# Kernel optimization log

Hardware: AMD Instinct MI355X
Metric: run time of the kernel (lower is better)

## Reference

```python
import jax, jax.numpy as jnp
import numpy as np

K = 8  # search_range in sample_wise_recolor
BIG = 1e30


def setup_inputs() -> dict:
    key = jax.random.key(0)
    ks = jax.random.split(key, 6)
    L, N = 16384, 10000  # L: upsampled candidate voxels (multiple of 8), N: target points
    pred_F = jax.random.normal(ks[0], (L,), jnp.float32)
    cand_xyz = jax.random.normal(ks[1], (L, 3), jnp.float32) * 50.0
    cand_rgb = jax.random.uniform(ks[2], (L, 3), jnp.float32)
    tgt_xyz = jax.random.normal(ks[3], (N, 3), jnp.float32) * 50.0
    tgt_rgb = jax.random.uniform(ks[4], (N, 3), jnp.float32)
    keep_target = jax.random.randint(ks[5], (L,), 0, 2, jnp.int32)
    return {"pred_F": pred_F, "cand_xyz": cand_xyz, "cand_rgb": cand_rgb,
            "tgt_xyz": tgt_xyz, "tgt_rgb": tgt_rgb, "keep_target": keep_target,
            "points_num": 8192}


def _get_keep(pred, points_num):
    # local-max mask over groups of 8 children (scatter of per-row argmax)
    L = pred.shape[0]
    p8 = pred.reshape(-1, 8)
    rows = jnp.arange(p8.shape[0])
    is_local_max = jnp.zeros(p8.shape, dtype=bool).at[rows, jnp.argmax(p8, axis=1)].set(True).reshape(-1)
    # kthvalue over the non-local-max subset: local-max entries pushed to +inf so the
    # k-th smallest of the full sorted array equals the k-th smallest of the subset.
    k = L - points_num  # static python int
    vals = jnp.where(is_local_max, jnp.inf, pred)
    threshold = jnp.sort(vals)[k - 1]
    return (pred > threshold) | is_local_max


def _pairwise_sqdist(a, b):
    # a: [P,3], b: [Q,3] -> [P,Q] squared distances
    a2 = jnp.sum(a * a, axis=1)
    b2 = jnp.sum(b * b, axis=1)
    d2 = a2[:, None] + b2[None, :] - 2.0 * (a @ b.T)
    return jnp.maximum(d2, 0.0)


def _recolor_loss(cand_xyz, rgb, keep, tgt_xyz, tgt_rgb):
    L = cand_xyz.shape[0]
    N = tgt_xyz.shape[0]
    d2 = _pairwise_sqdist(tgt_xyz, cand_xyz)  # [N, L]

    # ---- recolor_backward: KNN from each target point into kept candidates ----
    d_masked = jnp.where(keep[None, :], d2, BIG)
    neg_d, idx = jax.lax.top_k(-d_masked, K)  # [N, K]
    d = -neg_d
    zero_mask = d == 0.0
    min_mask = (d == jnp.min(d, axis=1, keepdims=True)) & ~jnp.any(zero_mask, axis=1)[:, None]
    w = jnp.where(min_mask, 1.0 / jnp.sqrt(jnp.maximum(d, 1e-30)), 0.0)  # [N, K]

    flat_idx = idx.reshape(-1)
    num = jnp.zeros((L, 3), rgb.dtype).at[flat_idx].add((tgt_rgb[:, None, :] * w[:, :, None]).reshape(-1, 3))
    den = jnp.zeros((L,), rgb.dtype).at[flat_idx].add(w.reshape(-1))
    has_den = den != 0.0
    recolored = jnp.where(has_den[:, None], num / jnp.where(has_den, den, 1.0)[:, None], 0.0)

    # exact-match (zero-distance) targets overwrite; scatter with safe out-of-range dummy row
    safe_idx = jnp.where(zero_mask, idx, L).reshape(-1)
    tgt_exp = jnp.broadcast_to(tgt_rgb[:, None, :], (N, K, 3)).reshape(-1, 3)
    recolored = jnp.concatenate([recolored, jnp.zeros((1, 3), rgb.dtype)], 0).at[safe_idx].set(tgt_exp)[:L]
    empty = jnp.concatenate([~has_den, jnp.zeros((1,), bool)], 0).at[safe_idx].set(False)[:L]
    empty = empty & keep  # only kept candidates matter

    # ---- recolor_forward: kept candidates with no color yet pull from nearest targets ----
    neg_df, idxf = jax.lax.top_k(-d2.T, K)  # [L, K]
    df = -neg_df
    mf = df == jnp.min(df, axis=1, keepdims=True)
    rec_fwd = jnp.sum(tgt_rgb[idxf] * mf[:, :, None], axis=1) / jnp.sum(mf, axis=1, keepdims=True).astype(rgb.dtype)
    recolored = jnp.where(empty[:, None], rec_fwd, recolored)

    # L1 loss over kept candidates only; recolor target is no-grad in the original
    recolored = jax.lax.stop_gradient(recolored)
    return jnp.sum(jnp.where(keep[:, None], jnp.abs(rgb - recolored), 0.0))


def reference(pred_F, cand_xyz, cand_rgb, tgt_xyz, tgt_rgb, keep_target, points_num):
    keep = _get_keep(jax.lax.stop_gradient(pred_F), points_num)  # @torch.no_grad
    # coord recon loss: BCE-with-logits, reduction='sum'
    t = keep_target.astype(pred_F.dtype)
    coord_loss = jnp.sum(jnp.maximum(pred_F, 0.0) - pred_F * t + jnp.log1p(jnp.exp(-jnp.abs(pred_F))))
    # inverse_transform_for_color in training mode: x * 255
    rgb = cand_rgb * 255.0
    rgb_loss = _recolor_loss(cand_xyz, rgb, keep, tgt_xyz, tgt_rgb)
    return jnp.stack([coord_loss, rgb_loss])
```

## Files before the change

### kernel.cpp

```cpp
#include <hip/hip_runtime.h>
#include <hip/hip_bf16.h>


#define SCAN_T 256
typedef unsigned long long ull;

__global__ __launch_bounds__(256) void k_prep(
    const float* __restrict__ pred, const float* __restrict__ txyz,
    float4* __restrict__ ttile, float4* __restrict__ numden,
    int* __restrict__ zerohit, ull* __restrict__ tmin, ull* __restrict__ fmin,
    unsigned int* __restrict__ key, unsigned char* __restrict__ islm,
    int* __restrict__ counters, float* __restrict__ out, int L, int N) {
  int gidx = blockIdx.x * 256 + threadIdx.x;
  int gsz = (int)gridDim.x * 256;
  for (int i = gidx; i < N; i += gsz) {
    float x = txyz[3*i], y = txyz[3*i+1], z = txyz[3*i+2];
    ttile[i] = make_float4(x, y, z, fmaf(x, x, fmaf(y, y, z * z)));
    tmin[i] = ~0ull;
  }
  for (int i = gidx; i < L; i += gsz) {
    numden[i] = make_float4(0.f, 0.f, 0.f, 0.f);
    zerohit[i] = 0;
    fmin[i] = ~0ull;
  }
  if (gidx < 8) counters[gidx] = 0;
  if (gidx < 2) out[gidx] = 0.f;
  int ngroups = L >> 3;
  for (int g = gidx; g < ngroups; g += gsz) {
    const float4* pv = (const float4*)pred + (size_t)g * 2;
    float4 a = pv[0], b = pv[1];
    float v[8] = {a.x, a.y, a.z, a.w, b.x, b.y, b.z, b.w};
    int bi = 0; float bv = v[0];
    #pragma unroll
    for (int j = 1; j < 8; ++j) if (v[j] > bv) { bv = v[j]; bi = j; }
    unsigned int kk[8];
    ull lmpack = 0ull;
    #pragma unroll
    for (int j = 0; j < 8; ++j) {
      unsigned int fb = __float_as_uint(v[j]);
      unsigned int mk = (fb & 0x80000000u) ? ~fb : (fb | 0x80000000u);
      if (j == bi) { mk = 0xFF800000u; lmpack |= 1ull << (8 * j); }
      kk[j] = mk;
    }
    ((uint4*)key)[g*2]   = make_uint4(kk[0], kk[1], kk[2], kk[3]);
    ((uint4*)key)[g*2+1] = make_uint4(kk[4], kk[5], kk[6], kk[7]);
    *(ull*)(islm + (size_t)g * 8) = lmpack;
  }
}

__device__ __forceinline__ void select_bin(
    unsigned int* hist, int nb, unsigned int rank,
    unsigned int* sB, unsigned int* sR, int tid) {
  if (tid < 64) {
    int g = nb >> 6;
    unsigned int sum = 0;
    for (int j = 0; j < g; ++j) sum += hist[tid * g + j];
    unsigned int incl = sum;
    for (int o = 1; o < 64; o <<= 1) {
      unsigned int v = __shfl_up(incl, o);
      if (tid >= o) incl += v;
    }
    unsigned int excl = incl - sum;
    bool cond = (rank >= excl) && (rank < incl);
    unsigned long long bal = __ballot(cond);
    int first = __ffsll((long long)bal) - 1;
    if (tid == first) {
      unsigned int r = rank - excl, cum = 0;
      for (int j = 0; j < g; ++j) {
        unsigned int c = hist[tid * g + j];
        if (r < cum + c) { *sB = (unsigned int)(tid * g + j); *sR = r - cum; break; }
        cum += c;
      }
    }
  }
}

__global__ __launch_bounds__(256) void k_sel(
    const unsigned int* __restrict__ key, const int* __restrict__ pnum_p,
    float* __restrict__ thr_out, int L) {
  __shared__ unsigned int hist[2048];
  __shared__ unsigned int sB, sR;
  int tid = threadIdx.x;
  unsigned int rank = (unsigned int)(L - pnum_p[0] - 1);
  const uint4* k4 = (const uint4*)key;
  int n4 = L >> 2;
  for (int b = tid; b < 2048; b += 256) hist[b] = 0u;
  __syncthreads();
  for (int i = tid; i < n4; i += 256) {
    uint4 v = k4[i];
    atomicAdd(&hist[v.x >> 21], 1u); atomicAdd(&hist[v.y >> 21], 1u);
    atomicAdd(&hist[v.z >> 21], 1u); atomicAdd(&hist[v.w >> 21], 1u);
  }
  __syncthreads();
  select_bin(hist, 2048, rank, &sB, &sR, tid);
  __syncthreads();
  unsigned int B1 = sB, R1 = sR;
  for (int b = tid; b < 2048; b += 256) hist[b] = 0u;
  __syncthreads();
  for (int i = tid; i < n4; i += 256) {
    uint4 v = k4[i];
    if ((v.x >> 21) == B1) atomicAdd(&hist[(v.x >> 10) & 2047u], 1u);
    if ((v.y >> 21) == B1) atomicAdd(&hist[(v.y >> 10) & 2047u], 1u);
    if ((v.z >> 21) == B1) atomicAdd(&hist[(v.z >> 10) & 2047u], 1u);
    if ((v.w >> 21) == B1) atomicAdd(&hist[(v.w >> 10) & 2047u], 1u);
  }
  __syncthreads();
  select_bin(hist, 2048, R1, &sB, &sR, tid);
  __syncthreads();
  unsigned int B2 = sB, R2 = sR;
  for (int b = tid; b < 1024; b += 256) hist[b] = 0u;
  __syncthreads();
  unsigned int top22 = (B1 << 11) | B2;
  for (int i = tid; i < n4; i += 256) {
    uint4 v = k4[i];
    if ((v.x >> 10) == top22) atomicAdd(&hist[v.x & 1023u], 1u);
    if ((v.y >> 10) == top22) atomicAdd(&hist[v.y & 1023u], 1u);
    if ((v.z >> 10) == top22) atomicAdd(&hist[v.z & 1023u], 1u);
    if ((v.w >> 10) == top22) atomicAdd(&hist[v.w & 1023u], 1u);
  }
  __syncthreads();
  select_bin(hist, 1024, R2, &sB, &sR, tid);
  __syncthreads();
  if (tid == 0) {
    unsigned int fkey = (B1 << 21) | (B2 << 10) | sB;
    unsigned int fb = (fkey & 0x80000000u) ? (fkey & 0x7FFFFFFFu) : ~fkey;
    thr_out[0] = __uint_as_float(fb);
  }
}

__global__ __launch_bounds__(256) void k_keepc(
    const float* __restrict__ pred, const unsigned char* __restrict__ islm,
    const float* __restrict__ thr_p, const float* __restrict__ cxyz,
    const int* __restrict__ ktgt, int* __restrict__ keep,
    float4* __restrict__ klist, int* __restrict__ kidx,
    int* __restrict__ counters, float* __restrict__ out, int L) {
  int i = blockIdx.x * 256 + threadIdx.x;
  float thr = thr_p[0];
  float term = 0.f;
  if (i < L) {
    float p = pred[i];
    bool kp = (p > thr) || islm[i];
    keep[i] = kp ? 1 : 0;
    if (kp) {
      int pos = atomicAdd(&counters[0], 1);
      float x = cxyz[3*i], y = cxyz[3*i+1], z = cxyz[3*i+2];
      klist[pos] = make_float4(x, y, z, fmaf(x, x, fmaf(y, y, z * z)));
      kidx[pos] = i;
    }
    float t = (float)ktgt[i];
    term = fmaxf(p, 0.f) - p * t + log1pf(expf(-fabsf(p)));
  }
  for (int o = 32; o > 0; o >>= 1) term += __shfl_down(term, o);
  if ((threadIdx.x & 63) == 0) atomicAdd(&out[0], term);
}

__global__ __launch_bounds__(SCAN_T) void k_scan2(
    const float* __restrict__ txyz, const float4* __restrict__ klist,
    const int* __restrict__ kidx, const float4* __restrict__ ttile,
    const int* __restrict__ counters, ull* __restrict__ tmin,
    ull* __restrict__ fmin, int L, int N, int YB) {
  __shared__ float4 tile[SCAN_T];
  int tid = threadIdx.x, x = blockIdx.x, y = blockIdx.y;
  int kc = counters[0];

  if (y < YB) {
    int c0 = y * 512;
    if (x * 256 >= N || c0 >= kc) return;
    int c1 = min(c0 + 512, kc);
    int t = x * 256 + tid;
    bool act = t < N;
    float tx = 0.f, ty = 0.f, tz = 0.f;
    if (act) { tx = txyz[3*t]; ty = txyz[3*t+1]; tz = txyz[3*t+2]; }
    float ntx = -2.f * tx, nty = -2.f * ty, ntz = -2.f * tz;
    float best = 3e38f; int bpos = -1;
    for (int tb = c0; tb < c1; tb += SCAN_T) {
      int cnt = min(SCAN_T, c1 - tb);
      if (tid < cnt) tile[tid] = klist[tb + tid];
      __syncthreads();
      #pragma unroll 8
      for (int c = 0; c < cnt; ++c) {
        float4 cd = tile[c];
        float d = fmaf(ntx, cd.x, cd.w);
        d = fmaf(nty, cd.y, d);
        d = fmaf(ntz, cd.z, d);
        if (d < best) { best = d; bpos = tb + c; }
      }
      __syncthreads();
    }
    if (act && bpos >= 0) {
      float4 cd = klist[bpos];
      float dx = tx - cd.x, dy = ty - cd.y, dz = tz - cd.z;
      float dtrue = fmaf(dx, dx, fmaf(dy, dy, dz * dz));
      ull pack = ((ull)__float_as_uint(dtrue) << 32) | (unsigned int)kidx[bpos];
      atomicMin(&tmin[t], pack);
    }
  } else {
    int t0 = (y - YB) * 512;
    if (x * 256 >= kc) return;
    int t1 = min(t0 + 512, N);
    int e = x * 256 + tid;
    bool act = e < kc;
    float cx = 0.f, cy = 0.f, cz = 0.f, c2 = 0.f;
    int l = 0;
    if (act) {
      float4 cd = klist[e];
      cx = cd.x; cy = cd.y; cz = cd.z; c2 = cd.w;
      l = kidx[e];
    }
    float ncx = -2.f * cx, ncy = -2.f * cy, ncz = -2.f * cz;
    float best = 3e38f; int bidx = 0;
    for (int tb = t0; tb < t1; tb += SCAN_T) {
      int cnt = min(SCAN_T, t1 - tb);
      if (tid < cnt) tile[tid] = ttile[tb + tid];
      __syncthreads();
      #pragma unroll 8
      for (int c = 0; c < cnt; ++c) {
        float4 td = tile[c];
        float d = fmaf(ncx, td.x, td.w);
        d = fmaf(ncy, td.y, d);
        d = fmaf(ncz, td.z, d);
        if (d < best) { best = d; bidx = tb + c; }
      }
      __syncthreads();
    }
    if (act) {
      float dkey = fmaxf(best + c2, 0.f);
      ull pack = ((ull)__float_as_uint(dkey) << 32) | (unsigned int)bidx;
      atomicMin(&fmin[l], pack);
    }
  }
}

__global__ __launch_bounds__(256) void k_scatter(
    const float* __restrict__ trgb, const ull* __restrict__ tmin,
    float4* __restrict__ numden, int* __restrict__ zerohit,
    float4* __restrict__ zcolor, int N) {
  int t = blockIdx.x * 256 + threadIdx.x;
  if (t >= N) return;
  ull pack = tmin[t];
  float d = __uint_as_float((unsigned int)(pack >> 32));
  int idx = (int)(pack & 0xFFFFFFFFull);
  float r = trgb[3*t], g = trgb[3*t+1], b = trgb[3*t+2];
  if (d == 0.0f) {
    zerohit[idx] = 1;
    zcolor[idx] = make_float4(r, g, b, 0.f);
  } else {
    float w = 1.0f / sqrtf(fmaxf(d, 1e-30f));
    atomicAdd(&numden[idx].x, r * w);
    atomicAdd(&numden[idx].y, g * w);
    atomicAdd(&numden[idx].z, b * w);
    atomicAdd(&numden[idx].w, w);
  }
}

__global__ __launch_bounds__(256) void k_loss(
    const float* __restrict__ crgb, const float* __restrict__ trgb,
    const int* __restrict__ keep, const float4* __restrict__ numden,
    const int* __restrict__ zerohit, const float4* __restrict__ zcolor,
    const ull* __restrict__ fmin, float* __restrict__ out, int L) {
  int l = blockIdx.x * 256 + threadIdx.x;
  float loss = 0.f;
  if (l < L && keep[l]) {
    float rr, rg, rb;
    if (zerohit[l]) {
      float4 z = zcolor[l]; rr = z.x; rg = z.y; rb = z.z;
    } else {
      float4 nd = numden[l];
      if (nd.w != 0.f) { rr = nd.x / nd.w; rg = nd.y / nd.w; rb = nd.z / nd.w; }
      else {
        int ti = (int)(fmin[l] & 0xFFFFFFFFull);
        rr = trgb[3*ti]; rg = trgb[3*ti+1]; rb = trgb[3*ti+2];
      }
    }
    float sr = crgb[3*l]*255.f, sg = crgb[3*l+1]*255.f, sb = crgb[3*l+2]*255.f;
    loss = fabsf(sr - rr) + fabsf(sg - rg) + fabsf(sb - rb);
  }
  for (int o = 32; o > 0; o >>= 1) loss += __shfl_down(loss, o);
  if ((threadIdx.x & 63) == 0) atomicAdd(&out[1], loss);
}

extern "C" void kernel_launch(void* const* d_in, const int* in_sizes, int n_in,
                              void* d_out, int out_size, void* d_ws, size_t ws_size,
                              hipStream_t stream) {
  const float* pred = (const float*)d_in[0];
  const float* cxyz = (const float*)d_in[1];
  const float* crgb = (const float*)d_in[2];
  const float* txyz = (const float*)d_in[3];
  const float* trgb = (const float*)d_in[4];
  const int*   ktgt = (const int*)d_in[5];
  const int*   pnum = (const int*)d_in[6];
  int L = in_sizes[0];
  int N = in_sizes[3] / 3;

  char* ws = (char*)d_ws;
  size_t off = 0;
  float4* klist  = (float4*)(ws + off);   off += (size_t)L * 16;
  float4* ttile  = (float4*)(ws + off);   off += (size_t)((N + 3) & ~3) * 16;
  float4* numden = (float4*)(ws + off);   off += (size_t)L * 16;
  float4* zcolor = (float4*)(ws + off);   off += (size_t)L * 16;
  unsigned int* key = (unsigned int*)(ws + off); off += (size_t)L * 4;
  ull* tmin      = (ull*)(ws + off);      off += (size_t)((N + 1) & ~1) * 8;
  ull* fmin      = (ull*)(ws + off);      off += (size_t)L * 8;
  int* keep      = (int*)(ws + off);      off += (size_t)L * 4;
  int* kidx      = (int*)(ws + off);      off += (size_t)L * 4;
  int* zerohit   = (int*)(ws + off);      off += (size_t)L * 4;
  float* thr_slot = (float*)(ws + off);   off += 16;
  int* counters  = (int*)(ws + off);      off += 256;
  unsigned char* islm = (unsigned char*)(ws + off); off += ((size_t)L + 15) & ~15ull;
  float* out = (float*)d_out;

  int nbL = (L + 255) / 256;
  int nbN = (N + 255) / 256;
  int YB = (L + 511) / 512;
  int YF = (N + 511) / 512;
  int mx = max(L, N);

  k_prep<<<(mx + 255) / 256, 256, 0, stream>>>(
      pred, txyz, ttile, numden, zerohit, tmin, fmin, key, islm, counters, out, L, N);

  k_sel<<<1, 256, 0, stream>>>(key, pnum, thr_slot, L);

  k_keepc<<<nbL, 256, 0, stream>>>(
      pred, islm, thr_slot, cxyz, ktgt, keep, klist, kidx, counters, out, L);

  dim3 gs(nbL, YB + YF);
  k_scan2<<<gs, SCAN_T, 0, stream>>>(
      txyz, klist, kidx, ttile, counters, tmin, fmin, L, N, YB);

  k_scatter<<<nbN, 256, 0, stream>>>(trgb, tmin, numden, zerohit, zcolor, N);

  k_loss<<<nbL, 256, 0, stream>>>(
      crgb, trgb, keep, numden, zerohit, zcolor, fmin, out, L);
}
```

Baseline: 141.4 us.

## Register-block four queries per thread in brute-force nearest-neighbour scan

Each thread in the pairwise nearest-neighbour scan now tracks four query points instead of one, so every shared-memory tile element is reused four times. Each block also loads a single 256-element tile instead of looping over 512. The grid is reshaped to give 1024 queries by 256 references per block. This cuts LDS reads and per-block loop overhead per distance evaluation, at the cost of more registers, fewer blocks in x, and more atomicMin operations because the reference chunks are smaller.

```diff
diff --git a/kernel.cpp b/kernel.cpp
--- a/kernel.cpp
+++ b/kernel.cpp
@@ -164,69 +164,90 @@
   int kc = counters[0];
 
   if (y < YB) {
-    int c0 = y * 512;
-    if (x * 256 >= N || c0 >= kc) return;
-    int c1 = min(c0 + 512, kc);
-    int t = x * 256 + tid;
-    bool act = t < N;
-    float tx = 0.f, ty = 0.f, tz = 0.f;
-    if (act) { tx = txyz[3*t]; ty = txyz[3*t+1]; tz = txyz[3*t+2]; }
-    float ntx = -2.f * tx, nty = -2.f * ty, ntz = -2.f * tz;
-    float best = 3e38f; int bpos = -1;
-    for (int tb = c0; tb < c1; tb += SCAN_T) {
-      int cnt = min(SCAN_T, c1 - tb);
-      if (tid < cnt) tile[tid] = klist[tb + tid];
-      __syncthreads();
-      #pragma unroll 8
-      for (int c = 0; c < cnt; ++c) {
-        float4 cd = tile[c];
-        float d = fmaf(ntx, cd.x, cd.w);
-        d = fmaf(nty, cd.y, d);
-        d = fmaf(ntz, cd.z, d);
-        if (d < best) { best = d; bpos = tb + c; }
-      }
-      __syncthreads();
-    }
-    if (act && bpos >= 0) {
-      float4 cd = klist[bpos];
-      float dx = tx - cd.x, dy = ty - cd.y, dz = tz - cd.z;
-      float dtrue = fmaf(dx, dx, fmaf(dy, dy, dz * dz));
-      ull pack = ((ull)__float_as_uint(dtrue) << 32) | (unsigned int)kidx[bpos];
-      atomicMin(&tmin[t], pack);
+    int c0 = y * SCAN_T;
+    if (x * 1024 >= N || c0 >= kc) return;
+    int cnt = min(SCAN_T, kc - c0);
+    if (tid < cnt) tile[tid] = klist[c0 + tid];
+    __syncthreads();
+    int tb = x * 1024 + tid;
+    float ntx[4], nty[4], ntz[4], best[4];
+    int bpos[4];
+    bool act[4];
+    #pragma unroll
+    for (int j = 0; j < 4; ++j) {
+      int t = tb + 256 * j;
+      act[j] = t < N;
+      float tx = 0.f, ty = 0.f, tz = 0.f;
+      if (act[j]) { tx = txyz[3*t]; ty = txyz[3*t+1]; tz = txyz[3*t+2]; }
+      ntx[j] = -2.f * tx; nty[j] = -2.f * ty; ntz[j] = -2.f * tz;
+      best[j] = 3e38f; bpos[j] = 0;
+    }
+    #pragma unroll 4
+    for (int c = 0; c < cnt; ++c) {
+      float4 cd = tile[c];
+      #pragma unroll
+      for (int j = 0; j < 4; ++j) {
+        float d = fmaf(ntx[j], cd.x, cd.w);
+        d = fmaf(nty[j], cd.y, d);
+        d = fmaf(ntz[j], cd.z, d);
+        if (d < best[j]) { best[j] = d; bpos[j] = c; }
+      }
+    }
+    #pragma unroll
+    for (int j = 0; j < 4; ++j) {
+      if (act[j]) {
+        int p = c0 + bpos[j];
+        float4 cd = klist[p];
+        float tx = -0.5f * ntx[j], ty = -0.5f * nty[j], tz = -0.5f * ntz[j];
+        float dx = tx - cd.x, dy = ty - cd.y, dz = tz - cd.z;
+        float dtrue = fmaf(dx, dx, fmaf(dy, dy, dz * dz));
+        ull pack = ((ull)__float_as_uint(dtrue) << 32) | (unsigned int)kidx[p];
+        atomicMin(&tmin[tb + 256 * j], pack);
+      }
     }
   } else {
-    int t0 = (y - YB) * 512;
-    if (x * 256 >= kc) return;
-    int t1 = min(t0 + 512, N);
-    int e = x * 256 + tid;
-    bool act = e < kc;
-    float cx = 0.f, cy = 0.f, cz = 0.f, c2 = 0.f;
-    int l = 0;
-    if (act) {
-      float4 cd = klist[e];
-      cx = cd.x; cy = cd.y; cz = cd.z; c2 = cd.w;
-      l = kidx[e];
-    }
-    float ncx = -2.f * cx, ncy = -2.f * cy, ncz = -2.f * cz;
-    float best = 3e38f; int bidx = 0;
-    for (int tb = t0; tb < t1; tb += SCAN_T) {
-      int cnt = min(SCAN_T, t1 - tb);
-      if (tid < cnt) tile[tid] = ttile[tb + tid];
-      __syncthreads();
-      #pragma unroll 8
-      for (int c = 0; c < cnt; ++c) {
-        float4 td = tile[c];
-        float d = fmaf(ncx, td.x, td.w);
-        d = fmaf(ncy, td.y, d);
-        d = fmaf(ncz, td.z, d);
-        if (d < best) { best = d; bidx = tb + c; }
-      }
-      __syncthreads();
-    }
-    if (act) {
-      float dkey = fmaxf(best + c2, 0.f);
-      ull pack = ((ull)__float_as_uint(dkey) << 32) | (unsigned int)bidx;
-      atomicMin(&fmin[l], pack);
+    int t0 = (y - YB) * SCAN_T;
+    if (x * 1024 >= kc || t0 >= N) return;
+    int tcnt = min(SCAN_T, N - t0);
+    if (tid < tcnt) tile[tid] = ttile[t0 + tid];
+    __syncthreads();
+    int eb = x * 1024 + tid;
+    float ncx[4], ncy[4], ncz[4], c2[4], best[4];
+    int bpos[4], li[4];
+    bool act[4];
+    #pragma unroll
+    for (int j = 0; j < 4; ++j) {
+      int e = eb + 256 * j;
+      act[j] = e < kc;
+      float cx = 0.f, cy = 0.f, cz = 0.f;
+      c2[j] = 0.f; li[j] = 0;
+      if (act[j]) {
+        float4 cd = klist[e];
+        cx = cd.x; cy = cd.y; cz = cd.z; c2[j] = cd.w;
+        li[j] = kidx[e];
+      }
+      ncx[j] = -2.f * cx; ncy[j] = -2.f * cy; ncz[j] = -2.f * cz;
+      best[j] = 3e38f; bpos[j] = 0;
+    }
+    #pragma unroll 4
+    for (int c = 0; c < tcnt; ++c) {
+      float4 td = tile[c];
+      #pragma unroll
+      for (int j = 0; j < 4; ++j) {
+        float d = fmaf(ncx[j], td.x, td.w);
+        d = fmaf(ncy[j], td.y, d);
+        d = fmaf(ncz[j], td.z, d);
+        if (d < best[j]) { best[j] = d; bpos[j] = c; }
+      }
+    }
+    #pragma unroll
+    for (int j = 0; j < 4; ++j) {
+      if (act[j]) {
+        float dkey = fmaxf(best[j] + c2[j], 0.f);
+        ull pack = ((ull)__float_as_uint(dkey) << 32) |
+                   (unsigned int)(t0 + bpos[j]);
+        atomicMin(&fmin[li[j]], pack);
+      }
     }
   }
 }
@@ -311,8 +332,6 @@
 
   int nbL = (L + 255) / 256;
   int nbN = (N + 255) / 256;
-  int YB = (L + 511) / 512;
-  int YF = (N + 511) / 512;
   int mx = max(L, N);
 
   k_prep<<<(mx + 255) / 256, 256, 0, stream>>>(
@@ -323,7 +342,10 @@
   k_keepc<<<nbL, 256, 0, stream>>>(
       pred, islm, thr_slot, cxyz, ktgt, keep, klist, kidx, counters, out, L);
 
-  dim3 gs(nbL, YB + YF);
+  int gx = (mx + 1023) / 1024;
+  int YB = (L + SCAN_T - 1) / SCAN_T;
+  int YF = (N + SCAN_T - 1) / SCAN_T;
+  dim3 gs(gx, YB + YF);
   k_scan2<<<gs, SCAN_T, 0, stream>>>(
       txyz, klist, kidx, ttile, counters, tmin, fmin, L, N, YB);
 
```

After: 144.5 us. 2.2% more time.

## Fuse init with selection and reduce NN search in-block to drop atomics and scatter kernel

Applied to the files above, without the earlier changes.

Merges the prep and threshold-selection kernels into one launch. The selection block builds its radix keys in shared memory instead of global memory. The nearest-neighbour scan now gives each block 32 queries and splits the candidate axis across 8 thread groups, then takes the minimum in shared memory. This removes the global atomicMin buffers and the separate scatter kernel, and the scatter is done inline after the reduction. In exchange, each block walks the full candidate or target list and only 32 threads hold each query, so the per-block scan is longer and block count changes. The single selection block now runs serially alongside the init blocks.

```diff
diff --git a/kernel.cpp b/kernel.cpp
--- a/kernel.cpp
+++ b/kernel.cpp
@@ -2,51 +2,7 @@
 #include <hip/hip_bf16.h>
 
 
-#define SCAN_T 256
 typedef unsigned long long ull;
-
-__global__ __launch_bounds__(256) void k_prep(
-    const float* __restrict__ pred, const float* __restrict__ txyz,
-    float4* __restrict__ ttile, float4* __restrict__ numden,
-    int* __restrict__ zerohit, ull* __restrict__ tmin, ull* __restrict__ fmin,
-    unsigned int* __restrict__ key, unsigned char* __restrict__ islm,
-    int* __restrict__ counters, float* __restrict__ out, int L, int N) {
-  int gidx = blockIdx.x * 256 + threadIdx.x;
-  int gsz = (int)gridDim.x * 256;
-  for (int i = gidx; i < N; i += gsz) {
-    float x = txyz[3*i], y = txyz[3*i+1], z = txyz[3*i+2];
-    ttile[i] = make_float4(x, y, z, fmaf(x, x, fmaf(y, y, z * z)));
-    tmin[i] = ~0ull;
-  }
-  for (int i = gidx; i < L; i += gsz) {
-    numden[i] = make_float4(0.f, 0.f, 0.f, 0.f);
-    zerohit[i] = 0;
-    fmin[i] = ~0ull;
-  }
-  if (gidx < 8) counters[gidx] = 0;
-  if (gidx < 2) out[gidx] = 0.f;
-  int ngroups = L >> 3;
-  for (int g = gidx; g < ngroups; g += gsz) {
-    const float4* pv = (const float4*)pred + (size_t)g * 2;
-    float4 a = pv[0], b = pv[1];
-    float v[8] = {a.x, a.y, a.z, a.w, b.x, b.y, b.z, b.w};
-    int bi = 0; float bv = v[0];
-    #pragma unroll
-    for (int j = 1; j < 8; ++j) if (v[j] > bv) { bv = v[j]; bi = j; }
-    unsigned int kk[8];
-    ull lmpack = 0ull;
-    #pragma unroll
-    for (int j = 0; j < 8; ++j) {
-      unsigned int fb = __float_as_uint(v[j]);
-      unsigned int mk = (fb & 0x80000000u) ? ~fb : (fb | 0x80000000u);
-      if (j == bi) { mk = 0xFF800000u; lmpack |= 1ull << (8 * j); }
-      kk[j] = mk;
-    }
-    ((uint4*)key)[g*2]   = make_uint4(kk[0], kk[1], kk[2], kk[3]);
-    ((uint4*)key)[g*2+1] = make_uint4(kk[4], kk[5], kk[6], kk[7]);
-    *(ull*)(islm + (size_t)g * 8) = lmpack;
-  }
-}
 
 __device__ __forceinline__ void select_bin(
     unsigned int* hist, int nb, unsigned int rank,
@@ -75,19 +31,62 @@
   }
 }
 
-__global__ __launch_bounds__(256) void k_sel(
-    const unsigned int* __restrict__ key, const int* __restrict__ pnum_p,
-    float* __restrict__ thr_out, int L) {
+__global__ __launch_bounds__(512) void k_init_sel(
+    const float* __restrict__ pred, const float* __restrict__ txyz,
+    const int* __restrict__ pnum_p,
+    float4* __restrict__ ttile, float4* __restrict__ numden,
+    int* __restrict__ zerohit,
+    unsigned char* __restrict__ islm, int* __restrict__ counters,
+    float* __restrict__ out, float* __restrict__ thr_out,
+    int L, int N, int IB) {
+  __shared__ unsigned int skey[16384];
   __shared__ unsigned int hist[2048];
   __shared__ unsigned int sB, sR;
   int tid = threadIdx.x;
+
+  if ((int)blockIdx.x < IB) {
+    int gidx = blockIdx.x * 512 + tid;
+    int gsz = IB * 512;
+    for (int i = gidx; i < N; i += gsz) {
+      float x = txyz[3*i], y = txyz[3*i+1], z = txyz[3*i+2];
+      ttile[i] = make_float4(x, y, z, fmaf(x, x, fmaf(y, y, z * z)));
+    }
+    for (int i = gidx; i < L; i += gsz) {
+      numden[i] = make_float4(0.f, 0.f, 0.f, 0.f);
+      zerohit[i] = 0;
+    }
+    if (gidx < 8) counters[gidx] = 0;
+    if (gidx < 2) out[gidx] = 0.f;
+    return;
+  }
+
+  int ngroups = L >> 3;
+  for (int g = tid; g < ngroups; g += 512) {
+    const float4* pv = (const float4*)pred + (size_t)g * 2;
+    float4 a = pv[0], b = pv[1];
+    float v[8] = {a.x, a.y, a.z, a.w, b.x, b.y, b.z, b.w};
+    int bi = 0; float bv = v[0];
+    #pragma unroll
+    for (int j = 1; j < 8; ++j) if (v[j] > bv) { bv = v[j]; bi = j; }
+    ull lmpack = 0ull;
+    #pragma unroll
+    for (int j = 0; j < 8; ++j) {
+      unsigned int fb = __float_as_uint(v[j]);
+      unsigned int mk = (fb & 0x80000000u) ? ~fb : (fb | 0x80000000u);
+      if (j == bi) { mk = 0xFF800000u; lmpack |= 1ull << (8 * j); }
+      skey[g * 8 + j] = mk;
+    }
+    *(ull*)(islm + (size_t)g * 8) = lmpack;
+  }
+  __syncthreads();
+
   unsigned int rank = (unsigned int)(L - pnum_p[0] - 1);
-  const uint4* k4 = (const uint4*)key;
+  const uint4* s4 = (const uint4*)skey;
   int n4 = L >> 2;
-  for (int b = tid; b < 2048; b += 256) hist[b] = 0u;
-  __syncthreads();
-  for (int i = tid; i < n4; i += 256) {
-    uint4 v = k4[i];
+  for (int b = tid; b < 2048; b += 512) hist[b] = 0u;
+  __syncthreads();
+  for (int i = tid; i < n4; i += 512) {
+    uint4 v = s4[i];
     atomicAdd(&hist[v.x >> 21], 1u); atomicAdd(&hist[v.y >> 21], 1u);
     atomicAdd(&hist[v.z >> 21], 1u); atomicAdd(&hist[v.w >> 21], 1u);
   }
@@ -95,10 +94,10 @@
   select_bin(hist, 2048, rank, &sB, &sR, tid);
   __syncthreads();
   unsigned int B1 = sB, R1 = sR;
-  for (int b = tid; b < 2048; b += 256) hist[b] = 0u;
-  __syncthreads();
-  for (int i = tid; i < n4; i += 256) {
-    uint4 v = k4[i];
+  for (int b = tid; b < 2048; b += 512) hist[b] = 0u;
+  __syncthreads();
+  for (int i = tid; i < n4; i += 512) {
+    uint4 v = s4[i];
     if ((v.x >> 21) == B1) atomicAdd(&hist[(v.x >> 10) & 2047u], 1u);
     if ((v.y >> 21) == B1) atomicAdd(&hist[(v.y >> 10) & 2047u], 1u);
     if ((v.z >> 21) == B1) atomicAdd(&hist[(v.z >> 10) & 2047u], 1u);
@@ -108,11 +107,11 @@
   select_bin(hist, 2048, R1, &sB, &sR, tid);
   __syncthreads();
   unsigned int B2 = sB, R2 = sR;
-  for (int b = tid; b < 1024; b += 256) hist[b] = 0u;
+  for (int b = tid; b < 1024; b += 512) hist[b] = 0u;
   __syncthreads();
   unsigned int top22 = (B1 << 11) | B2;
-  for (int i = tid; i < n4; i += 256) {
-    uint4 v = k4[i];
+  for (int i = tid; i < n4; i += 512) {
+    uint4 v = s4[i];
     if ((v.x >> 10) == top22) atomicAdd(&hist[v.x & 1023u], 1u);
     if ((v.y >> 10) == top22) atomicAdd(&hist[v.y & 1023u], 1u);
     if ((v.z >> 10) == top22) atomicAdd(&hist[v.z & 1023u], 1u);
@@ -154,31 +153,36 @@
   if ((threadIdx.x & 63) == 0) atomicAdd(&out[0], term);
 }
 
-__global__ __launch_bounds__(SCAN_T) void k_scan2(
-    const float* __restrict__ txyz, const float4* __restrict__ klist,
-    const int* __restrict__ kidx, const float4* __restrict__ ttile,
-    const int* __restrict__ counters, ull* __restrict__ tmin,
-    ull* __restrict__ fmin, int L, int N, int YB) {
-  __shared__ float4 tile[SCAN_T];
-  int tid = threadIdx.x, x = blockIdx.x, y = blockIdx.y;
+__global__ __launch_bounds__(256) void k_scan2(
+    const float* __restrict__ txyz, const float* __restrict__ trgb,
+    const float4* __restrict__ klist, const int* __restrict__ kidx,
+    const float4* __restrict__ ttile, const int* __restrict__ counters,
+    float4* __restrict__ numden, int* __restrict__ zerohit,
+    float4* __restrict__ zcolor, ull* __restrict__ fmin,
+    int L, int N, int BB) {
+  __shared__ float4 tile[256];
+  __shared__ ull red[4][32];
+  int tid = threadIdx.x, bx = blockIdx.x;
   int kc = counters[0];
-
-  if (y < YB) {
-    int c0 = y * 512;
-    if (x * 256 >= N || c0 >= kc) return;
-    int c1 = min(c0 + 512, kc);
-    int t = x * 256 + tid;
+  int lane = tid & 63, wv = tid >> 6;
+  int tgt = tid & 31;
+  int lo = (tid >> 5) * 32;
+
+  if (bx < BB) {
+    int T0 = bx * 32;
+    int t = T0 + tgt;
     bool act = t < N;
     float tx = 0.f, ty = 0.f, tz = 0.f;
     if (act) { tx = txyz[3*t]; ty = txyz[3*t+1]; tz = txyz[3*t+2]; }
     float ntx = -2.f * tx, nty = -2.f * ty, ntz = -2.f * tz;
     float best = 3e38f; int bpos = -1;
-    for (int tb = c0; tb < c1; tb += SCAN_T) {
-      int cnt = min(SCAN_T, c1 - tb);
+    for (int tb = 0; tb < kc; tb += 256) {
+      int cnt = min(256, kc - tb);
       if (tid < cnt) tile[tid] = klist[tb + tid];
       __syncthreads();
-      #pragma unroll 8
-      for (int c = 0; c < cnt; ++c) {
+      int hi = min(lo + 32, cnt);
+      #pragma unroll 4
+      for (int c = lo; c < hi; ++c) {
         float4 cd = tile[c];
         float d = fmaf(ntx, cd.x, cd.w);
         d = fmaf(nty, cd.y, d);
@@ -187,69 +191,80 @@
       }
       __syncthreads();
     }
+    ull pack = ~0ull;
     if (act && bpos >= 0) {
       float4 cd = klist[bpos];
       float dx = tx - cd.x, dy = ty - cd.y, dz = tz - cd.z;
       float dtrue = fmaf(dx, dx, fmaf(dy, dy, dz * dz));
-      ull pack = ((ull)__float_as_uint(dtrue) << 32) | (unsigned int)kidx[bpos];
-      atomicMin(&tmin[t], pack);
+      pack = ((ull)__float_as_uint(dtrue) << 32) | (unsigned int)kidx[bpos];
+    }
+    ull o = __shfl_down(pack, 32);
+    pack = (o < pack) ? o : pack;
+    if (lane < 32) red[wv][lane] = pack;
+    __syncthreads();
+    if (wv == 0 && lane < 32 && act) {
+      ull m = red[0][lane];
+      ull m1 = red[1][lane]; m = (m1 < m) ? m1 : m;
+      ull m2 = red[2][lane]; m = (m2 < m) ? m2 : m;
+      ull m3 = red[3][lane]; m = (m3 < m) ? m3 : m;
+      float d = __uint_as_float((unsigned int)(m >> 32));
+      int idx = (int)(m & 0xFFFFFFFFull);
+      float r = trgb[3*t], g = trgb[3*t+1], b = trgb[3*t+2];
+      if (d == 0.0f) {
+        zerohit[idx] = 1;
+        zcolor[idx] = make_float4(r, g, b, 0.f);
+      } else {
+        float w = 1.0f / sqrtf(fmaxf(d, 1e-30f));
+        atomicAdd(&numden[idx].x, r * w);
+        atomicAdd(&numden[idx].y, g * w);
+        atomicAdd(&numden[idx].z, b * w);
+        atomicAdd(&numden[idx].w, w);
+      }
     }
   } else {
-    int t0 = (y - YB) * 512;
-    if (x * 256 >= kc) return;
-    int t1 = min(t0 + 512, N);
-    int e = x * 256 + tid;
+    int C0 = (bx - BB) * 32;
+    if (C0 >= kc) return;
+    int e = C0 + tgt;
     bool act = e < kc;
-    float cx = 0.f, cy = 0.f, cz = 0.f, c2 = 0.f;
-    int l = 0;
+    float ncx = 0.f, ncy = 0.f, ncz = 0.f, c2 = 0.f;
+    int li = 0;
     if (act) {
       float4 cd = klist[e];
-      cx = cd.x; cy = cd.y; cz = cd.z; c2 = cd.w;
-      l = kidx[e];
-    }
-    float ncx = -2.f * cx, ncy = -2.f * cy, ncz = -2.f * cz;
-    float best = 3e38f; int bidx = 0;
-    for (int tb = t0; tb < t1; tb += SCAN_T) {
-      int cnt = min(SCAN_T, t1 - tb);
+      ncx = -2.f * cd.x; ncy = -2.f * cd.y; ncz = -2.f * cd.z;
+      c2 = cd.w; li = kidx[e];
+    }
+    float best = 3e38f; int bpos = -1;
+    for (int tb = 0; tb < N; tb += 256) {
+      int cnt = min(256, N - tb);
       if (tid < cnt) tile[tid] = ttile[tb + tid];
       __syncthreads();
-      #pragma unroll 8
-      for (int c = 0; c < cnt; ++c) {
+      int hi = min(lo + 32, cnt);
+      #pragma unroll 4
+      for (int c = lo; c < hi; ++c) {
         float4 td = tile[c];
         float d = fmaf(ncx, td.x, td.w);
         d = fmaf(ncy, td.y, d);
         d = fmaf(ncz, td.z, d);
-        if (d < best) { best = d; bidx = tb + c; }
+        if (d < best) { best = d; bpos = tb + c; }
       }
       __syncthreads();
     }
-    if (act) {
+    ull pack = ~0ull;
+    if (act && bpos >= 0) {
       float dkey = fmaxf(best + c2, 0.f);
-      ull pack = ((ull)__float_as_uint(dkey) << 32) | (unsigned int)bidx;
-      atomicMin(&fmin[l], pack);
-    }
-  }
-}
-
-__global__ __launch_bounds__(256) void k_scatter(
-    const float* __restrict__ trgb, const ull* __restrict__ tmin,
-    float4* __restrict__ numden, int* __restrict__ zerohit,
-    float4* __restrict__ zcolor, int N) {
-  int t = blockIdx.x * 256 + threadIdx.x;
-  if (t >= N) return;
-  ull pack = tmin[t];
-  float d = __uint_as_float((unsigned int)(pack >> 32));
-  int idx = (int)(pack & 0xFFFFFFFFull);
-  float r = trgb[3*t], g = trgb[3*t+1], b = trgb[3*t+2];
-  if (d == 0.0f) {
-    zerohit[idx] = 1;
-    zcolor[idx] = make_float4(r, g, b, 0.f);
-  } else {
-    float w = 1.0f / sqrtf(fmaxf(d, 1e-30f));
-    atomicAdd(&numden[idx].x, r * w);
-    atomicAdd(&numden[idx].y, g * w);
-    atomicAdd(&numden[idx].z, b * w);
-    atomicAdd(&numden[idx].w, w);
+      pack = ((ull)__float_as_uint(dkey) << 32) | (unsigned int)bpos;
+    }
+    ull o = __shfl_down(pack, 32);
+    pack = (o < pack) ? o : pack;
+    if (lane < 32) red[wv][lane] = pack;
+    __syncthreads();
+    if (wv == 0 && lane < 32 && act) {
+      ull m = red[0][lane];
+      ull m1 = red[1][lane]; m = (m1 < m) ? m1 : m;
+      ull m2 = red[2][lane]; m = (m2 < m) ? m2 : m;
+      ull m3 = red[3][lane]; m = (m3 < m) ? m3 : m;
+      fmin[li] = m;
+    }
   }
 }
 
@@ -298,8 +313,6 @@
   float4* ttile  = (float4*)(ws + off);   off += (size_t)((N + 3) & ~3) * 16;
   float4* numden = (float4*)(ws + off);   off += (size_t)L * 16;
   float4* zcolor = (float4*)(ws + off);   off += (size_t)L * 16;
-  unsigned int* key = (unsigned int*)(ws + off); off += (size_t)L * 4;
-  ull* tmin      = (ull*)(ws + off);      off += (size_t)((N + 1) & ~1) * 8;
   ull* fmin      = (ull*)(ws + off);      off += (size_t)L * 8;
   int* keep      = (int*)(ws + off);      off += (size_t)L * 4;
   int* kidx      = (int*)(ws + off);      off += (size_t)L * 4;
@@ -310,24 +323,21 @@
   float* out = (float*)d_out;
 
   int nbL = (L + 255) / 256;
-  int nbN = (N + 255) / 256;
-  int YB = (L + 511) / 512;
-  int YF = (N + 511) / 512;
   int mx = max(L, N);
 
-  k_prep<<<(mx + 255) / 256, 256, 0, stream>>>(
-      pred, txyz, ttile, numden, zerohit, tmin, fmin, key, islm, counters, out, L, N);
-
-  k_sel<<<1, 256, 0, stream>>>(key, pnum, thr_slot, L);
+  int IB = (mx + 511) / 512;
+  k_init_sel<<<IB + 1, 512, 0, stream>>>(
+      pred, txyz, pnum, ttile, numden, zerohit, islm, counters,
+      out, thr_slot, L, N, IB);
 
   k_keepc<<<nbL, 256, 0, stream>>>(
       pred, islm, thr_slot, cxyz, ktgt, keep, klist, kidx, counters, out, L);
 
-  dim3 gs(nbL, YB + YF);
-  k_scan2<<<gs, SCAN_T, 0, stream>>>(
-      txyz, klist, kidx, ttile, counters, tmin, fmin, L, N, YB);
-
-  k_scatter<<<nbN, 256, 0, stream>>>(trgb, tmin, numden, zerohit, zcolor, N);
+  int BB = (N + 31) / 32;
+  int BF = (L + 31) / 32;
+  k_scan2<<<BB + BF, 256, 0, stream>>>(
+      txyz, trgb, klist, kidx, ttile, counters, numden, zerohit, zcolor,
+      fmin, L, N, BB);
 
   k_loss<<<nbL, 256, 0, stream>>>(
       crgb, trgb, keep, numden, zerohit, zcolor, fmin, out, L);
```

Result: slower. 148.6 us (+5.1%).
